# Kernel optimization log

Hardware: AMD Instinct MI355X
Metric: run time of the kernel (lower is better)

Reference implementation:

```python
import jax, jax.numpy as jnp
import numpy as np

B, L, DM = 4, 1024, 2048
H, KV, HD = 32, 4, 128
G = H // KV
E, TOPK, MI = 16, 8, 128
EPS = 1e-6
THETA = 1e6


def rms_norm(x, w):
    return x * jax.lax.rsqrt(jnp.mean(x * x, axis=-1, keepdims=True) + EPS) * w


def rotate_half(x):
    x1, x2 = jnp.split(x, 2, axis=-1)
    return jnp.concatenate([-x2, x1], axis=-1)


def setup_inputs() -> dict:
    key = jax.random.key(0)
    ks = jax.random.split(key, 10)
    s = 0.02
    # RoPE tables: [L, HD] broadcast to [B, L, HD]
    inv_freq = 1.0 / (THETA ** (jnp.arange(0, HD, 2, dtype=jnp.float32) / HD))
    ang = jnp.arange(L, dtype=jnp.float32)[:, None] * inv_freq[None, :]
    emb = jnp.concatenate([ang, ang], axis=-1)
    cos = jnp.broadcast_to(jnp.cos(emb)[None], (B, L, HD)).astype(jnp.float32)
    sin = jnp.broadcast_to(jnp.sin(emb)[None], (B, L, HD)).astype(jnp.float32)
    return {
        "x": jax.random.normal(ks[0], (B, L, DM), jnp.float32),
        "cos": cos,
        "sin": sin,
        "norm_attn_w": jnp.ones((DM,), jnp.float32),
        "q_w": jax.random.normal(ks[1], (H * HD, DM), jnp.float32) * s,
        "k_w": jax.random.normal(ks[2], (KV * HD, DM), jnp.float32) * s,
        "v_w": jax.random.normal(ks[3], (KV * HD, DM), jnp.float32) * s,
        "qn_w": jnp.ones((HD,), jnp.float32),
        "kn_w": jnp.ones((HD,), jnp.float32),
        "o_w": jax.random.normal(ks[4], (DM, H * HD), jnp.float32) * s,
        "norm_mlp_w": jnp.ones((DM,), jnp.float32),
        "router_w": jax.random.normal(ks[5], (E, DM), jnp.float32) * s,
        "egw": jax.random.normal(ks[6], (E, MI, DM), jnp.float32) * s,
        "euw": jax.random.normal(ks[7], (E, MI, DM), jnp.float32) * s,
        "edw": jax.random.normal(ks[8], (E, DM, MI), jnp.float32) * s,
    }


def _layer(x, cos, sin, norm_attn_w, q_w, k_w, v_w, qn_w, kn_w, o_w,
           norm_mlp_w, router_w, egw, euw, edw):
    b, l, dm = x.shape
    # ---- attention sub-block ----
    h = rms_norm(x, norm_attn_w)
    q = rms_norm((h @ q_w.T).reshape(b, l, H, HD), qn_w).swapaxes(1, 2)   # [B,H,L,D]
    k = rms_norm((h @ k_w.T).reshape(b, l, KV, HD), kn_w).swapaxes(1, 2)  # [B,KV,L,D]
    v = (h @ v_w.T).reshape(b, l, KV, HD).swapaxes(1, 2)                  # [B,KV,L,D]
    c = cos[:, None]  # [B,1,L,D]
    s = sin[:, None]
    q = c * q + s * rotate_half(q)
    k = c * k + s * rotate_half(k)
    # GQA: repeat kv heads
    k = jnp.repeat(k, G, axis=1)  # [B,H,L,D]
    v = jnp.repeat(v, G, axis=1)
    scores = jnp.einsum("bhqd,bhkd->bhqk", q, k) / jnp.sqrt(jnp.float32(HD))
    causal = jnp.tril(jnp.ones((l, l), bool))
    scores = jnp.where(causal[None, None], scores, jnp.float32(-1e30))
    attn = jax.nn.softmax(scores, axis=-1)
    o = jnp.einsum("bhqk,bhkd->bhqd", attn, v).swapaxes(1, 2).reshape(b, l, H * HD)
    x = x + o @ o_w.T
    # ---- sparse MoE MLP ----
    hm = rms_norm(x, norm_mlp_w).reshape(b * l, dm)  # [N,DM]
    logits = hm @ router_w.T                          # [N,E]
    probs = jax.nn.softmax(logits.astype(jnp.float32), axis=-1)
    rw, sel = jax.lax.top_k(probs, TOPK)              # [N,TOPK]
    rw = (rw / rw.sum(axis=-1, keepdims=True)).astype(x.dtype)
    n = b * l
    # dense combine weights [N,E] (topk indices are unique per token)
    w_dense = jnp.zeros((n, E), x.dtype).at[jnp.arange(n)[:, None], sel].add(rw)

    def body(acc, inp):
        gw, uw, dw, we = inp  # gw/uw [MI,DM], dw [DM,MI], we [N]
        a = jax.nn.silu(hm @ gw.T) * (hm @ uw.T)      # [N,MI]
        return acc + (a @ dw.T) * we[:, None], None

    out, _ = jax.lax.scan(body, jnp.zeros_like(hm), (egw, euw, edw, w_dense.T))
    return x + out.reshape(b, l, dm)


def reference(x, cos, sin, norm_attn_w, q_w, k_w, v_w, qn_w, kn_w, o_w,
              norm_mlp_w, router_w, egw, euw, edw):
    return _layer(x, cos, sin, norm_attn_w, q_w, k_w, v_w, qn_w, kn_w, o_w,
                  norm_mlp_w, router_w, egw, euw, edw)
```

## Files before the change

kernel.cpp:

```cpp
#include <hip/hip_runtime.h>
#include <stdint.h>

typedef _Float16 f16x8 __attribute__((ext_vector_type(8)));
typedef _Float16 f16x4 __attribute__((ext_vector_type(4)));
typedef float    f32x4 __attribute__((ext_vector_type(4)));

__device__ __forceinline__ void load16_lds(const _Float16* g, _Float16* l) {
    __builtin_amdgcn_global_load_lds(
        (const __attribute__((address_space(1))) void*)g,
        (__attribute__((address_space(3))) void*)l, 16, 0, 0);
}

__global__ __launch_bounds__(256) void k_castall(
    const float* __restrict__ q, const float* __restrict__ k,
    const float* __restrict__ v, const float* __restrict__ o,
    const float* __restrict__ eg, const float* __restrict__ eu,
    const float* __restrict__ edw,
    const float* __restrict__ x, const float* __restrict__ nattn,
    _Float16* __restrict__ qkvw, _Float16* __restrict__ ow,
    _Float16* __restrict__ guw, _Float16* __restrict__ dwc,
    _Float16* __restrict__ ones16, _Float16* __restrict__ h)
{
    const int bid = blockIdx.x;
    if (bid < 18432) {
        size_t i = ((size_t)bid * 256 + threadIdx.x) * 4;
        const float* src; _Float16* dst;
        if (i < 8388608)        { src = q + i;             dst = qkvw + i; }
        else if (i < 9437184)   { src = k + (i - 8388608); dst = qkvw + i; }
        else if (i < 10485760)  { src = v + (i - 9437184); dst = qkvw + i; }
        else                    { src = o + (i - 10485760); dst = ow + (i - 10485760); }
        float4 xx = *reinterpret_cast<const float4*>(src);
        f16x4 y = { (_Float16)xx.x, (_Float16)xx.y, (_Float16)xx.z, (_Float16)xx.w };
        *reinterpret_cast<f16x4*>(dst) = y;
    } else if (bid < 22528) {
        const int row = bid - 18432;
        const int e = row >> 8, rem = row & 255, half = rem >> 7, mi = rem & 127;
        const float* src = (half ? eu : eg) + ((size_t)(e * 128 + mi)) * 2048;
        const int c = threadIdx.x * 8;
        float4 v0 = *reinterpret_cast<const float4*>(src + c);
        float4 v1 = *reinterpret_cast<const float4*>(src + c + 4);
        f16x8 ov = { (_Float16)v0.x,(_Float16)v0.y,(_Float16)v0.z,(_Float16)v0.w,
                     (_Float16)v1.x,(_Float16)v1.y,(_Float16)v1.z,(_Float16)v1.w };
        *reinterpret_cast<f16x8*>(guw + (size_t)row * 2048 + c) = ov;
    } else if (bid < 26624) {
        int t = (bid - 22528) * 256 + threadIdx.x;
        int mi4 = (t & 31) * 4;
        int dm = (t >> 5) & 2047;
        int e = t >> 16;
        float4 vv = *reinterpret_cast<const float4*>(edw + (((size_t)e * 2048 + dm) << 7) + mi4);
        f16x4 ov = { (_Float16)vv.x, (_Float16)vv.y, (_Float16)vv.z, (_Float16)vv.w };
        *reinterpret_cast<f16x4*>(dwc + ((size_t)dm << 11) + e * 128 + mi4) = ov;
    } else if (bid == 26624) {
        int i = threadIdx.x;
        _Float16 vv = (i < 16) ? (_Float16)1.0f : (_Float16)0.0f;
        f16x4 ov = { vv, vv, vv, vv };
        *reinterpret_cast<f16x4*>(ones16 + i * 4) = ov;
    } else {
        const int row = bid - 26625, tid = threadIdx.x;
        const float* xr = x + (size_t)row * 2048;
        float4 a = *reinterpret_cast<const float4*>(xr + tid * 8);
        float4 b = *reinterpret_cast<const float4*>(xr + tid * 8 + 4);
        float ss = a.x*a.x + a.y*a.y + a.z*a.z + a.w*a.w
                 + b.x*b.x + b.y*b.y + b.z*b.z + b.w*b.w;
        #pragma unroll
        for (int m = 1; m < 64; m <<= 1) ss += __shfl_xor(ss, m);
        __shared__ float red[4];
        if ((tid & 63) == 0) red[tid >> 6] = ss;
        __syncthreads();
        float tot = red[0] + red[1] + red[2] + red[3];
        float r = rsqrtf(tot * (1.f / 2048.f) + 1e-6f);
        float4 wa = *reinterpret_cast<const float4*>(nattn + tid * 8);
        float4 wb = *reinterpret_cast<const float4*>(nattn + tid * 8 + 4);
        f16x8 hv = { (_Float16)(a.x*r*wa.x), (_Float16)(a.y*r*wa.y),
                     (_Float16)(a.z*r*wa.z), (_Float16)(a.w*r*wa.w),
                     (_Float16)(b.x*r*wb.x), (_Float16)(b.y*r*wb.y),
                     (_Float16)(b.z*r*wb.z), (_Float16)(b.w*r*wb.w) };
        *reinterpret_cast<f16x8*>(h + (size_t)row * 2048 + tid * 8) = hv;
    }
}

__global__ __launch_bounds__(256) void k_gemm(
    const _Float16* __restrict__ A, int lda,
    const _Float16* __restrict__ W, int ldw,
    float* __restrict__ Cf, _Float16* __restrict__ Ch, int ldc,
    const float* __restrict__ resid, int K)
{
    __shared__ __align__(16) _Float16 As[3][128][32];
    __shared__ __align__(16) _Float16 Ws[3][128][32];
    const int r0 = blockIdx.x * 128, c0 = blockIdx.y * 128;
    const int tid = threadIdx.x, lane = tid & 63, wid = tid >> 6;
    const int wr = wid >> 1, wc = wid & 1;
    const int sr = lane >> 2;
    const int scs = ((lane & 3) ^ ((lane >> 3) & 3)) * 8;
    const int fr = lane & 15;
    const int rks = (((lane >> 4) ^ ((fr >> 1) & 3))) * 8;
    const f32x4 z4 = { 0.f, 0.f, 0.f, 0.f };
    f32x4 acc[4][4];
    #pragma unroll
    for (int i = 0; i < 4; i++)
        #pragma unroll
        for (int j = 0; j < 4; j++) acc[i][j] = z4;

    auto stage = [&](int bf, int k0) {
        #pragma unroll
        for (int i = 0; i < 2; i++) {
            int ch = wid * 2 + i;
            load16_lds(A + (size_t)(r0 + ch * 16 + sr) * lda + k0 + scs, &As[bf][ch * 16][0]);
            load16_lds(W + (size_t)(c0 + ch * 16 + sr) * ldw + k0 + scs, &Ws[bf][ch * 16][0]);
        }
    };

    const int nt = K >> 5;
    stage(0, 0);
    if (nt > 1) stage(1, 32);
    int cur = 0;
    for (int t = 0; t < nt; t++) {
        if (t < nt - 1) asm volatile("s_waitcnt vmcnt(4)" ::: "memory");
        else            asm volatile("s_waitcnt vmcnt(0)" ::: "memory");
        __builtin_amdgcn_s_barrier();
        f16x8 af[4], bf4[4];
        #pragma unroll
        for (int i = 0; i < 4; i++)
            af[i] = *reinterpret_cast<const f16x8*>(&As[cur][wr * 64 + i * 16 + fr][rks]);
        #pragma unroll
        for (int j = 0; j < 4; j++)
            bf4[j] = *reinterpret_cast<const f16x8*>(&Ws[cur][wc * 64 + j * 16 + fr][rks]);
        if (t + 2 < nt) stage((t + 2) % 3, (t + 2) << 5);
        __builtin_amdgcn_s_setprio(1);
        #pragma unroll
        for (int i = 0; i < 4; i++)
            #pragma unroll
            for (int j = 0; j < 4; j++)
                acc[i][j] = __builtin_amdgcn_mfma_f32_16x16x32_f16(af[i], bf4[j], acc[i][j], 0, 0, 0);
        __builtin_amdgcn_s_setprio(0);
        cur = (cur + 1) % 3;
    }
    #pragma unroll
    for (int i = 0; i < 4; i++) {
        const int rowb = r0 + wr * 64 + i * 16 + (lane >> 4) * 4;
        #pragma unroll
        for (int j = 0; j < 4; j++) {
            const int col = c0 + wc * 64 + j * 16 + fr;
            #pragma unroll
            for (int r = 0; r < 4; r++) {
                size_t idx = (size_t)(rowb + r) * ldc + col;
                float v = acc[i][j][r];
                if (resid) v += resid[idx];
                if (Ch) Ch[idx] = (_Float16)v;
                else    Cf[idx] = v;
            }
        }
    }
}

__global__ __launch_bounds__(512, 2) void k_gemm8(
    const _Float16* __restrict__ A, int lda,
    const _Float16* __restrict__ W, int ldw,
    _Float16* __restrict__ Ch, int ldc, int K,
    const float* __restrict__ wdense, _Float16* __restrict__ ab)
{
    __shared__ __align__(16) _Float16 As[3][256][32];
    __shared__ __align__(16) _Float16 Ws[3][256][32];
    const int r0 = blockIdx.x * 256, c0 = blockIdx.y * 256;
    const int tid = threadIdx.x, lane = tid & 63, wid = tid >> 6;
    const int wr = wid >> 2, wc = wid & 3;
    const int rA = lane >> 2;
    const int scs = ((lane & 3) ^ ((lane >> 3) & 3)) * 8;
    const int fr = lane & 15, fg = lane >> 4;
    const int rks = (((lane >> 4) ^ ((fr >> 1) & 3))) * 8;
    const f32x4 z4 = { 0.f, 0.f, 0.f, 0.f };
    f32x4 acc[8][4];
    #pragma unroll
    for (int i = 0; i < 8; i++)
        #pragma unroll
        for (int j = 0; j < 4; j++) acc[i][j] = z4;

    auto stage = [&](int bf, int k0) {
        #pragma unroll
        for (int i = 0; i < 2; i++) {
            load16_lds(A + (size_t)(r0 + i * 128 + wid * 16 + rA) * lda + k0 + scs,
                       &As[bf][i * 128 + wid * 16][0]);
            load16_lds(W + (size_t)(c0 + i * 128 + wid * 16 + rA) * ldw + k0 + scs,
                       &Ws[bf][i * 128 + wid * 16][0]);
        }
    };

    const int nt = K >> 5;
    stage(0, 0);
    if (nt > 1) stage(1, 32);
    int cur = 0;
    for (int t = 0; t < nt; t++) {
        if (t < nt - 1) asm volatile("s_waitcnt vmcnt(4)" ::: "memory");
        else            asm volatile("s_waitcnt vmcnt(0)" ::: "memory");
        __builtin_amdgcn_s_barrier();
        f16x8 af[8], bf4[4];
        #pragma unroll
        for (int i = 0; i < 8; i++)
            af[i] = *reinterpret_cast<const f16x8*>(&As[cur][wr * 128 + i * 16 + fr][rks]);
        #pragma unroll
        for (int j = 0; j < 4; j++)
            bf4[j] = *reinterpret_cast<const f16x8*>(&Ws[cur][wc * 64 + j * 16 + fr][rks]);
        if (t + 2 < nt) stage((t + 2) % 3, (t + 2) << 5);
        __builtin_amdgcn_s_setprio(1);
        #pragma unroll
        for (int i = 0; i < 8; i++)
            #pragma unroll
            for (int j = 0; j < 4; j++)
                acc[i][j] = __builtin_amdgcn_mfma_f32_16x16x32_f16(af[i], bf4[j], acc[i][j], 0, 0, 0);
        __builtin_amdgcn_s_setprio(0);
        cur = (cur + 1) % 3;
    }

    if (!wdense) {
        #pragma unroll
        for (int i = 0; i < 8; i++) {
            const int rowb = r0 + wr * 128 + i * 16 + fg * 4;
            #pragma unroll
            for (int j = 0; j < 4; j++) {
                const int col = c0 + wc * 64 + j * 16 + fr;
                #pragma unroll
                for (int r = 0; r < 4; r++)
                    Ch[(size_t)(rowb + r) * ldc + col] = (_Float16)acc[i][j][r];
            }
        }
        return;
    }

    _Float16* LgA = &As[0][0][0];
    _Float16* LgB = &Ws[0][0][0];
    auto lgp = [&](int row, int mi) -> _Float16* {
        return ((row < 128) ? LgA : LgB) + (size_t)(row & 127) * 136 + mi;
    };
    const int e = blockIdx.y;
    __syncthreads();
    if (wc < 2) {
        #pragma unroll
        for (int i = 0; i < 8; i++) {
            const int row = wr * 128 + i * 16 + fg * 4;
            #pragma unroll
            for (int j = 0; j < 4; j++) {
                const int mi = wc * 64 + j * 16 + fr;
                #pragma unroll
                for (int r = 0; r < 4; r++)
                    *lgp(row + r, mi) = (_Float16)acc[i][j][r];
            }
        }
    }
    __syncthreads();
    if (wc >= 2) {
        #pragma unroll
        for (int i = 0; i < 8; i++) {
            const int row = wr * 128 + i * 16 + fg * 4;
            #pragma unroll
            for (int j = 0; j < 4; j++) {
                const int mi = (wc - 2) * 64 + j * 16 + fr;
                #pragma unroll
                for (int r = 0; r < 4; r++) {
                    float g = (float)*lgp(row + r, mi);
                    float sil = g / (1.f + __expf(-g));
                    *lgp(row + r, mi) = (_Float16)(sil * acc[i][j][r]);
                }
            }
        }
    }
    __syncthreads();
    #pragma unroll
    for (int pass = 0; pass < 8; pass++) {
        int cid = pass * 512 + tid;
        int row = cid >> 4, col8 = cid & 15;
        f16x8 v = *reinterpret_cast<const f16x8*>(
            ((row < 128) ? LgA : LgB) + (size_t)(row & 127) * 136 + col8 * 8);
        float wv = wdense[(size_t)e * 4096 + r0 + row];
        f16x8 o;
        #pragma unroll
        for (int j = 0; j < 8; j++) o[j] = (_Float16)((float)v[j] * wv);
        *reinterpret_cast<f16x8*>(ab + (size_t)(r0 + row) * 2048 + e * 128 + col8 * 8) = o;
    }
}

__global__ __launch_bounds__(256) void k_qkv_post(
    const _Float16* __restrict__ qkv,
    const float* __restrict__ cosb, const float* __restrict__ sinb,
    const float* __restrict__ qn_w, const float* __restrict__ kn_w,
    _Float16* __restrict__ qh, _Float16* __restrict__ kh,
    _Float16* __restrict__ vth)
{
    if (blockIdx.y == 9) {
        const int unit = blockIdx.x;
        if (unit >= 512) return;
        const int bkv = unit >> 5, rem = unit & 31;
        const int l0 = (rem >> 1) * 64, d0 = (rem & 1) * 64;
        const int b = bkv >> 2, kv = bkv & 3;
        __shared__ _Float16 T[64][72];
        const int t = threadIdx.x;
        const int r = t >> 3, c8 = (t & 7) * 8;
        #pragma unroll
        for (int rr = 0; rr < 2; rr++) {
            int l = l0 + r + rr * 32;
            *reinterpret_cast<f16x8*>(&T[r + rr * 32][c8]) =
                *reinterpret_cast<const f16x8*>(
                    qkv + (size_t)(b * 1024 + l) * 5120 + 4608 + kv * 128 + d0 + c8);
        }
        __syncthreads();
        #pragma unroll
        for (int rr = 0; rr < 2; rr++) {
            int d = d0 + r + rr * 32;
            f16x8 v;
            #pragma unroll
            for (int j = 0; j < 8; j++) v[j] = T[c8 + j][r + rr * 32];
            *reinterpret_cast<f16x8*>(vth + ((size_t)(bkv * 128 + d)) * 1024 + l0 + c8) = v;
        }
        return;
    }
    const int tok = blockIdx.x;
    const int u = blockIdx.y * 4 + (threadIdx.x >> 6);
    const int lane = threadIdx.x & 63;
    const int b = tok >> 10, l = tok & 1023;
    const float SCL = 0.12752887074166638f;
    const float c0 = cosb[(size_t)tok * 128 + lane];
    const float c1 = cosb[(size_t)tok * 128 + lane + 64];
    const float s0 = sinb[(size_t)tok * 128 + lane];
    const float s1 = sinb[(size_t)tok * 128 + lane + 64];
    if (u < 32) {
        const _Float16* base = qkv + (size_t)tok * 5120 + u * 128;
        float v0 = (float)base[lane], v1 = (float)base[lane + 64];
        float ss = v0 * v0 + v1 * v1;
        #pragma unroll
        for (int m = 1; m < 64; m <<= 1) ss += __shfl_xor(ss, m);
        float rms = rsqrtf(ss * (1.f / 128.f) + 1e-6f);
        float n0 = v0 * rms * qn_w[lane], n1 = v1 * rms * qn_w[lane + 64];
        _Float16* o = qh + (size_t)tok * 4096 + u * 128;
        o[lane]      = (_Float16)(SCL * (c0 * n0 - s0 * n1));
        o[lane + 64] = (_Float16)(SCL * (c1 * n1 + s1 * n0));
    } else {
        const int kvh = u - 32;
        const _Float16* base = qkv + (size_t)tok * 5120 + 4096 + kvh * 128;
        float v0 = (float)base[lane], v1 = (float)base[lane + 64];
        float ss = v0 * v0 + v1 * v1;
        #pragma unroll
        for (int m = 1; m < 64; m <<= 1) ss += __shfl_xor(ss, m);
        float rms = rsqrtf(ss * (1.f / 128.f) + 1e-6f);
        float n0 = v0 * rms * kn_w[lane], n1 = v1 * rms * kn_w[lane + 64];
        _Float16* o = kh + (((size_t)(b * 4 + kvh)) * 1024 + l) * 128;
        o[lane]      = (_Float16)(c0 * n0 - s0 * n1);
        o[lane + 64] = (_Float16)(c1 * n1 + s1 * n0);
    }
}

__global__ __launch_bounds__(512) void k_attn(
    const _Float16* __restrict__ qh, const _Float16* __restrict__ kh,
    const _Float16* __restrict__ vth, const _Float16* __restrict__ ones16,
    _Float16* __restrict__ oh)
{
    const int bh = blockIdx.x;
    const int qb = 3 - blockIdx.y;
    const int b = bh >> 5, h = bh & 31, kv = h >> 3;
    const int tid = threadIdx.x, lane = tid & 63, wid = tid >> 6;
    const int fr = lane & 15, fg = lane >> 4;
    const int q0w = qb * 256 + wid * 32;

    __shared__ __align__(16) _Float16 Ks[2][64][128];
    __shared__ __align__(16) _Float16 Vs[2][128][64];
    __shared__ __align__(16) _Float16 Vones[16][64];
    __shared__ __align__(16) _Float16 Ps[8][32][72];

    const _Float16* kb = kh + ((size_t)(b * 4 + kv)) * 1024 * 128;
    const _Float16* vb = vth + ((size_t)(b * 4 + kv)) * 128 * 1024;

    auto stage = [&](int nb, int key0) {
        #pragma unroll
        for (int i = 0; i < 2; i++) {
            int rr = wid * 8 + i * 4 + (lane >> 4);
            int c16 = (lane & 15) ^ (rr & 15);
            load16_lds(kb + (size_t)(key0 + rr) * 128 + c16 * 8,
                       &Ks[nb][0][0] + (wid * 8 + i * 4) * 128);
        }
        #pragma unroll
        for (int i = 0; i < 2; i++) {
            int rr = wid * 16 + i * 8 + (lane >> 3);
            int c16 = (lane & 7) ^ (rr & 7);
            load16_lds(vb + (size_t)rr * 1024 + key0 + c16 * 8,
                       &Vs[nb][0][0] + (wid * 16 + i * 8) * 64);
        }
    };

    f16x8 aq[2][4];
    #pragma unroll
    for (int mi = 0; mi < 2; mi++) {
        const _Float16* qbase =
            qh + ((size_t)(b * 1024 + q0w + mi * 16 + fr)) * 4096 + h * 128;
        #pragma unroll
        for (int kk = 0; kk < 4; kk++)
            aq[mi][kk] = *reinterpret_cast<const f16x8*>(qbase + kk * 32 + fg * 8);
    }
    if (wid == 0) {
        #pragma unroll
        for (int i = 0; i < 2; i++)
            load16_lds(ones16 + (size_t)(lane + i * 64) * 8, &Vones[0][0] + i * 512);
    }
    stage(0, 0);

    const f32x4 z4 = { 0.f, 0.f, 0.f, 0.f };
    f32x4 oacc[2][9];
    #pragma unroll
    for (int mi = 0; mi < 2; mi++)
        #pragma unroll
        for (int dj = 0; dj < 9; dj++) oacc[mi][dj] = z4;

    const int ntiles = qb * 4 + 4;
    int cb = 0;
    for (int kt = 0; kt < ntiles; kt++) {
        const int key0 = kt * 64;
        asm volatile("s_waitcnt vmcnt(0)" ::: "memory");
        __builtin_amdgcn_s_barrier();
        if (kt + 1 < ntiles) stage(cb ^ 1, key0 + 64);

        if (key0 <= q0w + 31) {
            f32x4 sc[2][4];
            #pragma unroll
            for (int mi = 0; mi < 2; mi++)
                #pragma unroll
                for (int j = 0; j < 4; j++) sc[mi][j] = z4;
            __builtin_amdgcn_s_setprio(1);
            #pragma unroll
            for (int j = 0; j < 4; j++)
                #pragma unroll
                for (int kk = 0; kk < 4; kk++) {
                    f16x8 bk = *reinterpret_cast<const f16x8*>(
                        &Ks[cb][0][0] + (j * 16 + fr) * 128 + (((kk * 4 + fg) ^ fr) * 8));
                    #pragma unroll
                    for (int mi = 0; mi < 2; mi++)
                        sc[mi][j] = __builtin_amdgcn_mfma_f32_16x16x32_f16(
                            aq[mi][kk], bk, sc[mi][j], 0, 0, 0);
                }
            __builtin_amdgcn_s_setprio(0);

            const bool maskt = (key0 + 63 > q0w);
            #pragma unroll
            for (int mi = 0; mi < 2; mi++)
                #pragma unroll
                for (int j = 0; j < 4; j++) {
                    const int key = key0 + j * 16 + fr;
                    #pragma unroll
                    for (int r = 0; r < 4; r++) {
                        float v = sc[mi][j][r];
                        if (maskt && key > q0w + mi * 16 + fg * 4 + r) v = -1e30f;
                        Ps[wid][mi * 16 + fg * 4 + r][j * 16 + fr] =
                            (_Float16)__builtin_amdgcn_exp2f(v - 8.f);
                    }
                }

            __builtin_amdgcn_s_setprio(1);
            #pragma unroll
            for (int ks = 0; ks < 2; ks++) {
                f16x8 ap0 = *reinterpret_cast<const f16x8*>(
                    &Ps[wid][fr][ks * 32 + fg * 8]);
                f16x8 ap1 = *reinterpret_cast<const f16x8*>(
                    &Ps[wid][16 + fr][ks * 32 + fg * 8]);
                #pragma unroll
                for (int dj = 0; dj < 8; dj++) {
                    f16x8 bv = *reinterpret_cast<const f16x8*>(
                        &Vs[cb][0][0] + (dj * 16 + fr) * 64 + (((ks * 4 + fg) ^ (fr & 7)) * 8));
                    oacc[0][dj] = __builtin_amdgcn_mfma_f32_16x16x32_f16(ap0, bv, oacc[0][dj], 0, 0, 0);
                    oacc[1][dj] = __builtin_amdgcn_mfma_f32_16x16x32_f16(ap1, bv, oacc[1][dj], 0, 0, 0);
                }
                f16x8 bo = *reinterpret_cast<const f16x8*>(
                    &Vones[0][0] + fr * 64 + (((ks * 4 + fg) ^ (fr & 7)) * 8));
                oacc[0][8] = __builtin_amdgcn_mfma_f32_16x16x32_f16(ap0, bo, oacc[0][8], 0, 0, 0);
                oacc[1][8] = __builtin_amdgcn_mfma_f32_16x16x32_f16(ap1, bo, oacc[1][8], 0, 0, 0);
            }
            __builtin_amdgcn_s_setprio(0);
        }
        cb ^= 1;
    }

    #pragma unroll
    for (int mi = 0; mi < 2; mi++) {
        float inv[4];
        #pragma unroll
        for (int r = 0; r < 4; r++) {
            float l = __shfl(oacc[mi][8][r], lane & 48);
            inv[r] = 1.f / l;
        }
        #pragma unroll
        for (int dj = 0; dj < 8; dj++)
            #pragma unroll
            for (int r = 0; r < 4; r++)
                oh[((size_t)(b * 1024 + q0w + mi * 16 + fg * 4 + r)) * 4096
                   + h * 128 + dj * 16 + fr] = (_Float16)(oacc[mi][dj][r] * inv[r]);
    }
}

__global__ __launch_bounds__(256) void k_mlppre(
    const float* __restrict__ x2, const float* __restrict__ nmlp,
    const float* __restrict__ rw,
    _Float16* __restrict__ hm, float* __restrict__ wdense)
{
    const int bid = blockIdx.x;
    if (bid < 4096) {
        const int row = bid, tid = threadIdx.x;
        const float* xr = x2 + (size_t)row * 2048;
        float4 a = *reinterpret_cast<const float4*>(xr + tid * 8);
        float4 b = *reinterpret_cast<const float4*>(xr + tid * 8 + 4);
        float ss = a.x*a.x + a.y*a.y + a.z*a.z + a.w*a.w
                 + b.x*b.x + b.y*b.y + b.z*b.z + b.w*b.w;
        #pragma unroll
        for (int m = 1; m < 64; m <<= 1) ss += __shfl_xor(ss, m);
        __shared__ float red[4];
        if ((tid & 63) == 0) red[tid >> 6] = ss;
        __syncthreads();
        float tot = red[0] + red[1] + red[2] + red[3];
        float r = rsqrtf(tot * (1.f / 2048.f) + 1e-6f);
        float4 wa = *reinterpret_cast<const float4*>(nmlp + tid * 8);
        float4 wb = *reinterpret_cast<const float4*>(nmlp + tid * 8 + 4);
        f16x8 hv = { (_Float16)(a.x*r*wa.x), (_Float16)(a.y*r*wa.y),
                     (_Float16)(a.z*r*wa.z), (_Float16)(a.w*r*wa.w),
                     (_Float16)(b.x*r*wb.x), (_Float16)(b.y*r*wb.y),
                     (_Float16)(b.z*r*wb.z), (_Float16)(b.w*r*wb.w) };
        *reinterpret_cast<f16x8*>(hm + (size_t)row * 2048 + tid * 8) = hv;
        return;
    }
    const int tok = (bid - 4096) * 4 + (threadIdx.x >> 6);
    const int lane = threadIdx.x & 63;
    __shared__ float lg[4][16];
    const float* hr = x2 + (size_t)tok * 2048;
    float vals[32];
    float ss = 0.f;
    #pragma unroll
    for (int i = 0; i < 32; i++) { float v = hr[i * 64 + lane]; vals[i] = v; ss += v * v; }
    #pragma unroll
    for (int m = 1; m < 64; m <<= 1) ss += __shfl_xor(ss, m);
    float r = rsqrtf(ss * (1.f / 2048.f) + 1e-6f);
    #pragma unroll
    for (int i = 0; i < 32; i++) vals[i] *= r * nmlp[i * 64 + lane];
    for (int e = 0; e < 16; e++) {
        float acc = 0.f;
        #pragma unroll
        for (int i = 0; i < 32; i++) acc += vals[i] * rw[(size_t)e * 2048 + i * 64 + lane];
        #pragma unroll
        for (int m = 1; m < 64; m <<= 1) acc += __shfl_xor(acc, m);
        if (lane == 0) lg[threadIdx.x >> 6][e] = acc;
    }
    __syncthreads();
    if (lane == 0) {
        float* l = lg[threadIdx.x >> 6];
        float mx = l[0];
        for (int e = 1; e < 16; e++) mx = fmaxf(mx, l[e]);
        float p[16]; float sum = 0.f;
        for (int e = 0; e < 16; e++) { p[e] = expf(l[e] - mx); sum += p[e]; }
        for (int e = 0; e < 16; e++) p[e] /= sum;
        bool sel[16]; for (int e = 0; e < 16; e++) sel[e] = false;
        float ssum = 0.f;
        for (int t = 0; t < 8; t++) {
            int bi = -1; float bv = -1.f;
            for (int e = 0; e < 16; e++) if (!sel[e] && p[e] > bv) { bv = p[e]; bi = e; }
            sel[bi] = true; ssum += bv;
        }
        for (int e = 0; e < 16; e++)
            wdense[(size_t)e * 4096 + tok] = sel[e] ? p[e] / ssum : 0.f;
    }
}


extern "C" void kernel_launch(void* const* d_in, const int* in_sizes, int n_in,
                              void* d_out, int out_size, void* d_ws, size_t ws_size,
                              hipStream_t stream)
{
    const float* x        = (const float*)d_in[0];
    const float* cosb     = (const float*)d_in[1];
    const float* sinb     = (const float*)d_in[2];
    const float* nattn    = (const float*)d_in[3];
    const float* q_w      = (const float*)d_in[4];
    const float* k_w      = (const float*)d_in[5];
    const float* v_w      = (const float*)d_in[6];
    const float* qn_w     = (const float*)d_in[7];
    const float* kn_w     = (const float*)d_in[8];
    const float* o_w      = (const float*)d_in[9];
    const float* nmlp     = (const float*)d_in[10];
    const float* router_w = (const float*)d_in[11];
    const float* egw      = (const float*)d_in[12];
    const float* euw      = (const float*)d_in[13];
    const float* edw      = (const float*)d_in[14];

    char* w = (char*)d_ws;
    _Float16* qkvw_h = (_Float16*)(w + 0);
    _Float16* ow_h   = (_Float16*)(w + 20971520);
    _Float16* guw_h  = (_Float16*)(w + 37748736);
    _Float16* dwc_h  = (_Float16*)(w + 54525952);
    _Float16* h_h    = (_Float16*)(w + 62914560);
    _Float16* hm_h   = h_h;
    float*    x2     = (float*)(w + 79691776);
    _Float16* qkv_h  = (_Float16*)(w + 113246208);
    _Float16* o_h    = qkv_h;
    _Float16* ab_h   = qkv_h;
    _Float16* q_h    = (_Float16*)(w + 155189248);
    _Float16* k_h    = (_Float16*)(w + 188743680);
    _Float16* vt_h   = (_Float16*)(w + 192937984);
    float*    wdense = (float*)(w + 197132288);
    _Float16* ones_h = (_Float16*)(w + 197394432);

    k_castall<<<30721, 256, 0, stream>>>(q_w, k_w, v_w, o_w, egw, euw, edw, x, nattn,
                                         qkvw_h, ow_h, guw_h, dwc_h, ones_h, h_h);
    k_gemm8<<<dim3(16, 16), 512, 0, stream>>>(h_h, 2048, qkvw_h, 2048, qkv_h, 5120, 2048,
                                              nullptr, nullptr);
    k_gemm<<<dim3(32, 8), 256, 0, stream>>>(h_h, 2048, qkvw_h + (size_t)4096 * 2048, 2048,
                                            nullptr, qkv_h + 4096, 5120, nullptr, 2048);
    k_qkv_post<<<dim3(4096, 10), 256, 0, stream>>>(qkv_h, cosb, sinb, qn_w, kn_w,
                                                   q_h, k_h, vt_h);
    k_attn<<<dim3(128, 4), 512, 0, stream>>>(q_h, k_h, vt_h, ones_h, o_h);
    k_gemm<<<dim3(32, 16), 256, 0, stream>>>(o_h, 4096, ow_h, 4096,
                                             x2, nullptr, 2048, x, 4096);
    k_mlppre<<<5120, 256, 0, stream>>>(x2, nmlp, router_w, hm_h, wdense);
    k_gemm8<<<dim3(16, 16), 512, 0, stream>>>(hm_h, 2048, guw_h, 2048, nullptr, 0, 2048,
                                              wdense, ab_h);
    k_gemm<<<dim3(32, 16), 256, 0, stream>>>(ab_h, 2048, dwc_h, 2048,
                                             (float*)d_out, nullptr, 2048, x2, 2048);

    (void)in_sizes; (void)n_in; (void)out_size; (void)ws_size;
}
```

Measured before the change: 481.6 us.

## Split-K output projection on 256x256 GEMM with fused residual+RMSNorm epilogue

The o_proj GEMM (K=4096) now runs on the larger 256x256-tile k_gemm8 kernel with split-K of 2, writing two fp32 partial buffers. A new epilogue kernel sums the partials with the residual, writes x2, and computes the MLP RMSNorm fp16 output in one pass. The router becomes its own kernel. The goal is better MFMA tile efficiency and enough blocks to fill the GPU (16x8x2). The cost is extra fp32 partial traffic and one more launch. p1 aliases x2, which is safe only because each epilogue row reads p1 before writing x2 to the same addresses.

```diff
diff --git a/kernel.cpp b/kernel.cpp
--- a/kernel.cpp
+++ b/kernel.cpp
@@ -157,11 +157,13 @@
     const _Float16* __restrict__ A, int lda,
     const _Float16* __restrict__ W, int ldw,
     _Float16* __restrict__ Ch, int ldc, int K,
-    const float* __restrict__ wdense, _Float16* __restrict__ ab)
+    const float* __restrict__ wdense, _Float16* __restrict__ ab,
+    float* __restrict__ pf0, float* __restrict__ pf1)
 {
     __shared__ __align__(16) _Float16 As[3][256][32];
     __shared__ __align__(16) _Float16 Ws[3][256][32];
     const int r0 = blockIdx.x * 256, c0 = blockIdx.y * 256;
+    const size_t koff = (size_t)blockIdx.z * K;
     const int tid = threadIdx.x, lane = tid & 63, wid = tid >> 6;
     const int wr = wid >> 2, wc = wid & 3;
     const int rA = lane >> 2;
@@ -178,9 +180,9 @@
     auto stage = [&](int bf, int k0) {
         #pragma unroll
         for (int i = 0; i < 2; i++) {
-            load16_lds(A + (size_t)(r0 + i * 128 + wid * 16 + rA) * lda + k0 + scs,
+            load16_lds(A + (size_t)(r0 + i * 128 + wid * 16 + rA) * lda + koff + k0 + scs,
                        &As[bf][i * 128 + wid * 16][0]);
-            load16_lds(W + (size_t)(c0 + i * 128 + wid * 16 + rA) * ldw + k0 + scs,
+            load16_lds(W + (size_t)(c0 + i * 128 + wid * 16 + rA) * ldw + koff + k0 + scs,
                        &Ws[bf][i * 128 + wid * 16][0]);
         }
     };
@@ -211,6 +213,22 @@
         cur = (cur + 1) % 3;
     }
 
+    if (pf0) {
+        float* Cf = blockIdx.z ? pf1 : pf0;
+        #pragma unroll
+        for (int i = 0; i < 8; i++) {
+            const int rowb = r0 + wr * 128 + i * 16 + fg * 4;
+            #pragma unroll
+            for (int j = 0; j < 4; j++) {
+                const int col = c0 + wc * 64 + j * 16 + fr;
+                #pragma unroll
+                for (int r = 0; r < 4; r++)
+                    Cf[(size_t)(rowb + r) * ldc + col] = acc[i][j][r];
+            }
+        }
+        return;
+    }
+
     if (!wdense) {
         #pragma unroll
         for (int i = 0; i < 8; i++) {
@@ -276,6 +294,43 @@
         for (int j = 0; j < 8; j++) o[j] = (_Float16)((float)v[j] * wv);
         *reinterpret_cast<f16x8*>(ab + (size_t)(r0 + row) * 2048 + e * 128 + col8 * 8) = o;
     }
+}
+
+__global__ __launch_bounds__(256) void k_oepi(
+    const float* __restrict__ p0, const float* __restrict__ p1,
+    const float* __restrict__ x, const float* __restrict__ nmlp,
+    float* __restrict__ x2, _Float16* __restrict__ hm)
+{
+    const int row = blockIdx.x, tid = threadIdx.x;
+    const size_t base = (size_t)row * 2048 + tid * 8;
+    float4 a0 = *reinterpret_cast<const float4*>(p0 + base);
+    float4 a1 = *reinterpret_cast<const float4*>(p0 + base + 4);
+    float4 b0 = *reinterpret_cast<const float4*>(p1 + base);
+    float4 b1 = *reinterpret_cast<const float4*>(p1 + base + 4);
+    float4 c0 = *reinterpret_cast<const float4*>(x + base);
+    float4 c1 = *reinterpret_cast<const float4*>(x + base + 4);
+    float4 v0 = { a0.x + b0.x + c0.x, a0.y + b0.y + c0.y,
+                  a0.z + b0.z + c0.z, a0.w + b0.w + c0.w };
+    float4 v1 = { a1.x + b1.x + c1.x, a1.y + b1.y + c1.y,
+                  a1.z + b1.z + c1.z, a1.w + b1.w + c1.w };
+    float ss = v0.x*v0.x + v0.y*v0.y + v0.z*v0.z + v0.w*v0.w
+             + v1.x*v1.x + v1.y*v1.y + v1.z*v1.z + v1.w*v1.w;
+    #pragma unroll
+    for (int m = 1; m < 64; m <<= 1) ss += __shfl_xor(ss, m);
+    __shared__ float red[4];
+    if ((tid & 63) == 0) red[tid >> 6] = ss;
+    __syncthreads();
+    float tot = red[0] + red[1] + red[2] + red[3];
+    float r = rsqrtf(tot * (1.f / 2048.f) + 1e-6f);
+    *reinterpret_cast<float4*>(x2 + base) = v0;
+    *reinterpret_cast<float4*>(x2 + base + 4) = v1;
+    float4 wa = *reinterpret_cast<const float4*>(nmlp + tid * 8);
+    float4 wb = *reinterpret_cast<const float4*>(nmlp + tid * 8 + 4);
+    f16x8 hv = { (_Float16)(v0.x*r*wa.x), (_Float16)(v0.y*r*wa.y),
+                 (_Float16)(v0.z*r*wa.z), (_Float16)(v0.w*r*wa.w),
+                 (_Float16)(v1.x*r*wb.x), (_Float16)(v1.y*r*wb.y),
+                 (_Float16)(v1.z*r*wb.z), (_Float16)(v1.w*r*wb.w) };
+    *reinterpret_cast<f16x8*>(hm + (size_t)row * 2048 + tid * 8) = hv;
 }
 
 __global__ __launch_bounds__(256) void k_qkv_post(
@@ -491,36 +546,11 @@
     }
 }
 
-__global__ __launch_bounds__(256) void k_mlppre(
-    const float* __restrict__ x2, const float* __restrict__ nmlp,
-    const float* __restrict__ rw,
-    _Float16* __restrict__ hm, float* __restrict__ wdense)
-{
-    const int bid = blockIdx.x;
-    if (bid < 4096) {
-        const int row = bid, tid = threadIdx.x;
-        const float* xr = x2 + (size_t)row * 2048;
-        float4 a = *reinterpret_cast<const float4*>(xr + tid * 8);
-        float4 b = *reinterpret_cast<const float4*>(xr + tid * 8 + 4);
-        float ss = a.x*a.x + a.y*a.y + a.z*a.z + a.w*a.w
-                 + b.x*b.x + b.y*b.y + b.z*b.z + b.w*b.w;
-        #pragma unroll
-        for (int m = 1; m < 64; m <<= 1) ss += __shfl_xor(ss, m);
-        __shared__ float red[4];
-        if ((tid & 63) == 0) red[tid >> 6] = ss;
-        __syncthreads();
-        float tot = red[0] + red[1] + red[2] + red[3];
-        float r = rsqrtf(tot * (1.f / 2048.f) + 1e-6f);
-        float4 wa = *reinterpret_cast<const float4*>(nmlp + tid * 8);
-        float4 wb = *reinterpret_cast<const float4*>(nmlp + tid * 8 + 4);
-        f16x8 hv = { (_Float16)(a.x*r*wa.x), (_Float16)(a.y*r*wa.y),
-                     (_Float16)(a.z*r*wa.z), (_Float16)(a.w*r*wa.w),
-                     (_Float16)(b.x*r*wb.x), (_Float16)(b.y*r*wb.y),
-                     (_Float16)(b.z*r*wb.z), (_Float16)(b.w*r*wb.w) };
-        *reinterpret_cast<f16x8*>(hm + (size_t)row * 2048 + tid * 8) = hv;
-        return;
-    }
-    const int tok = (bid - 4096) * 4 + (threadIdx.x >> 6);
+__global__ __launch_bounds__(256) void k_router(
+    const float* __restrict__ x2, const float* __restrict__ wm,
+    const float* __restrict__ rw, float* __restrict__ wdense)
+{
+    const int tok = blockIdx.x * 4 + (threadIdx.x >> 6);
     const int lane = threadIdx.x & 63;
     __shared__ float lg[4][16];
     const float* hr = x2 + (size_t)tok * 2048;
@@ -532,7 +562,7 @@
     for (int m = 1; m < 64; m <<= 1) ss += __shfl_xor(ss, m);
     float r = rsqrtf(ss * (1.f / 2048.f) + 1e-6f);
     #pragma unroll
-    for (int i = 0; i < 32; i++) vals[i] *= r * nmlp[i * 64 + lane];
+    for (int i = 0; i < 32; i++) vals[i] *= r * wm[i * 64 + lane];
     for (int e = 0; e < 16; e++) {
         float acc = 0.f;
         #pragma unroll
@@ -590,10 +620,12 @@
     _Float16* h_h    = (_Float16*)(w + 62914560);
     _Float16* hm_h   = h_h;
     float*    x2     = (float*)(w + 79691776);
+    float*    p1_f   = x2;
     _Float16* qkv_h  = (_Float16*)(w + 113246208);
     _Float16* o_h    = qkv_h;
     _Float16* ab_h   = qkv_h;
     _Float16* q_h    = (_Float16*)(w + 155189248);
+    float*    p0_f   = (float*)(w + 155189248);
     _Float16* k_h    = (_Float16*)(w + 188743680);
     _Float16* vt_h   = (_Float16*)(w + 192937984);
     float*    wdense = (float*)(w + 197132288);
@@ -602,17 +634,19 @@
     k_castall<<<30721, 256, 0, stream>>>(q_w, k_w, v_w, o_w, egw, euw, edw, x, nattn,
                                          qkvw_h, ow_h, guw_h, dwc_h, ones_h, h_h);
     k_gemm8<<<dim3(16, 16), 512, 0, stream>>>(h_h, 2048, qkvw_h, 2048, qkv_h, 5120, 2048,
-                                              nullptr, nullptr);
+                                              nullptr, nullptr, nullptr, nullptr);
     k_gemm<<<dim3(32, 8), 256, 0, stream>>>(h_h, 2048, qkvw_h + (size_t)4096 * 2048, 2048,
                                             nullptr, qkv_h + 4096, 5120, nullptr, 2048);
     k_qkv_post<<<dim3(4096, 10), 256, 0, stream>>>(qkv_h, cosb, sinb, qn_w, kn_w,
                                                    q_h, k_h, vt_h);
     k_attn<<<dim3(128, 4), 512, 0, stream>>>(q_h, k_h, vt_h, ones_h, o_h);
-    k_gemm<<<dim3(32, 16), 256, 0, stream>>>(o_h, 4096, ow_h, 4096,
-                                             x2, nullptr, 2048, x, 4096);
-    k_mlppre<<<5120, 256, 0, stream>>>(x2, nmlp, router_w, hm_h, wdense);
+    k_gemm8<<<dim3(16, 8, 2), 512, 0, stream>>>(o_h, 4096, ow_h, 4096,
+                                                nullptr, 2048, 2048,
+                                                nullptr, nullptr, p0_f, p1_f);
+    k_oepi<<<4096, 256, 0, stream>>>(p0_f, p1_f, x, nmlp, x2, hm_h);
+    k_router<<<1024, 256, 0, stream>>>(x2, nmlp, router_w, wdense);
     k_gemm8<<<dim3(16, 16), 512, 0, stream>>>(hm_h, 2048, guw_h, 2048, nullptr, 0, 2048,
-                                              wdense, ab_h);
+                                              wdense, ab_h, nullptr, nullptr);
     k_gemm<<<dim3(32, 16), 256, 0, stream>>>(ab_h, 2048, dwc_h, 2048,
                                              (float*)d_out, nullptr, 2048, x2, 2048);
 
```

After: 480.5 us. Within noise of the previous version (-0.2%).
